# Kernel tuning notes

Hardware: AMD Instinct MI355X
Metric: run time of the kernel (lower is better)

Reference implementation:

```python
import jax, jax.numpy as jnp
import numpy as np

N_NODES = 50000
NEG_SLOPE = 0.2  # PyG GATConv default
EPS = 1e-16      # PyG softmax eps


def gat_conv(x, src, dst, W, a_s, a_d, b, n_nodes):
    """One PyG-style GATConv layer (concat heads). a_s/a_d: [H, C]."""
    H, C = a_s.shape
    h = (x @ W).reshape(n_nodes, H, C)                   # [N, H, C]
    al_s = jnp.sum(h * a_s[None], axis=-1)               # [N, H]
    al_d = jnp.sum(h * a_d[None], axis=-1)               # [N, H]
    e = jax.nn.leaky_relu(al_s[src] + al_d[dst], NEG_SLOPE)  # [E, H]
    # segment softmax over incoming edges of each destination node
    m = jax.ops.segment_max(e, dst, num_segments=n_nodes)
    m = jnp.where(jnp.isfinite(m), m, 0.0)
    ex = jnp.exp(e - m[dst])
    denom = jax.ops.segment_sum(ex, dst, num_segments=n_nodes)
    alpha = ex / (denom[dst] + EPS)                       # [E, H]
    out = jax.ops.segment_sum(alpha[:, :, None] * h[src], dst, num_segments=n_nodes)
    return out.reshape(n_nodes, H * C) + b                # concat heads + bias


def setup_inputs() -> dict:
    key = jax.random.key(0)
    ks = jax.random.split(key, 16)
    s = 0.05
    return {
        "x": jax.random.normal(ks[0], (N_NODES, 256), jnp.float32),
        "edge_index": jax.random.randint(ks[1], (2, 800000), 0, N_NODES, jnp.int64),
        "W1": jax.random.normal(ks[2], (256, 256), jnp.float32) * s,
        "as1": jax.random.normal(ks[3], (4, 64), jnp.float32) * s,
        "ad1": jax.random.normal(ks[4], (4, 64), jnp.float32) * s,
        "b1": jnp.zeros((256,), jnp.float32),
        "W2": jax.random.normal(ks[5], (256, 256), jnp.float32) * s,
        "as2": jax.random.normal(ks[6], (4, 64), jnp.float32) * s,
        "ad2": jax.random.normal(ks[7], (4, 64), jnp.float32) * s,
        "b2": jnp.zeros((256,), jnp.float32),
        "W3": jax.random.normal(ks[8], (256, 128), jnp.float32) * s,
        "as3": jax.random.normal(ks[9], (1, 128), jnp.float32) * s,
        "ad3": jax.random.normal(ks[10], (1, 128), jnp.float32) * s,
        "b3": jnp.zeros((128,), jnp.float32),
    }


def reference(x, edge_index, W1, as1, ad1, b1, W2, as2, ad2, b2, W3, as3, ad3, b3):
    n = x.shape[0]
    loop = jnp.arange(n, dtype=edge_index.dtype)
    src = jnp.concatenate([edge_index[0], loop])  # add_self_loops=True (PyG default)
    dst = jnp.concatenate([edge_index[1], loop])
    # F.dropout(p=0.6, training=False) -> identity in eval
    h = gat_conv(x, src, dst, W1, as1, ad1, b1, n)
    h = jax.nn.elu(h)  # gnn_act='elu'
    h = gat_conv(h, src, dst, W2, as2, ad2, b2, n)
    h = jax.nn.elu(h)
    h = gat_conv(h, src, dst, W3, as3, ad3, b3, n)
    return h
```

## Files before the change

### kernel.cpp

```cpp
#include <hip/hip_runtime.h>
#include <math.h>


#define NEG_SLOPE 0.2f
#define EPS_SM 1e-16f

typedef _Float16 half8 __attribute__((ext_vector_type(8)));
typedef _Float16 half4v __attribute__((ext_vector_type(4)));
typedef _Float16 half2v __attribute__((ext_vector_type(2)));
typedef float f32x4 __attribute__((ext_vector_type(4)));

__device__ __forceinline__ float wave_allred_sum(float v) {
#pragma unroll
    for (int o = 32; o > 0; o >>= 1) v += __shfl_xor(v, o, 64);
    return v;
}
__device__ __forceinline__ float4 lrelu4(float4 v) {
    v.x = (v.x < 0.f) ? NEG_SLOPE * v.x : v.x;
    v.y = (v.y < 0.f) ? NEG_SLOPE * v.y : v.y;
    v.z = (v.z < 0.f) ? NEG_SLOPE * v.z : v.z;
    v.w = (v.w < 0.f) ? NEG_SLOPE * v.w : v.w;
    return v;
}

__global__ void hist_kernel(const int* __restrict__ ei, int E, int N,
                            int* __restrict__ cnt) {
    int e = blockIdx.x * 256 + threadIdx.x;
    int ET = E + N;
    if (e >= ET) return;
    int dst = (e < E) ? ei[E + e] : (e - E);
    atomicAdd(&cnt[dst], 1);
}

__global__ void scan_block(const int* __restrict__ cnt, int n_cnt,
                           int* __restrict__ offs, int n_off,
                           int* __restrict__ bsums) {
    __shared__ int buf[1024];
    int gid = blockIdx.x * 1024 + threadIdx.x;
    int v = (gid < n_cnt) ? cnt[gid] : 0;
    buf[threadIdx.x] = v;
    __syncthreads();
#pragma unroll
    for (int off = 1; off < 1024; off <<= 1) {
        int t = (threadIdx.x >= off) ? buf[threadIdx.x - off] : 0;
        __syncthreads();
        buf[threadIdx.x] += t;
        __syncthreads();
    }
    if (gid < n_off) offs[gid] = buf[threadIdx.x] - v;
    if (threadIdx.x == 1023) bsums[blockIdx.x] = buf[1023];
}

__global__ void scan_sums(int* __restrict__ bsums, int nb) {
    int l = threadIdx.x;
    int v = (l < nb) ? bsums[l] : 0;
    int s = v;
#pragma unroll
    for (int o = 1; o < 64; o <<= 1) {
        int t = __shfl_up(s, o, 64);
        if (l >= o) s += t;
    }
    if (l < nb) bsums[l] = s - v;
}

__global__ void scan_add(int* __restrict__ offs, int n_off,
                         const int* __restrict__ bsums) {
    int gid = blockIdx.x * 1024 + threadIdx.x;
    if (gid < n_off) offs[gid] += bsums[blockIdx.x];
}

__global__ void fill_csr(const int* __restrict__ ei, int E, int N,
                         const int* __restrict__ offs, int* __restrict__ fil,
                         int* __restrict__ csr) {
    int e = blockIdx.x * 256 + threadIdx.x;
    int ET = E + N;
    if (e >= ET) return;
    int src, dst;
    if (e < E) { src = ei[e]; dst = ei[E + e]; }
    else       { src = dst = e - E; }
    int pos = offs[dst] + atomicAdd(&fil[dst], 1);
    csr[pos] = src;
}

__global__ void wcast_all(const float* __restrict__ W1,
                          const float* __restrict__ W2,
                          const float* __restrict__ W3,
                          _Float16* __restrict__ o1,
                          _Float16* __restrict__ o2,
                          _Float16* __restrict__ o3) {
    int i = blockIdx.x * 256 + threadIdx.x;
    const float* W; _Float16* o; int K = 256, N, s;
    if (i < 65536)        { W = W1; o = o1; N = 256; s = i; }
    else if (i < 131072)  { W = W2; o = o2; N = 256; s = i - 65536; }
    else if (i < 163840)  { W = W3; o = o3; N = 128; s = i - 131072; }
    else return;
    int n = s / K, k = s - n * K;
    o[s] = (_Float16)W[(size_t)k * N + n];
}

template <bool AF32, int ALMODE>
__global__ __launch_bounds__(256) void gemm_f16(
    const void* __restrict__ Ain, const _Float16* __restrict__ Bt,
    _Float16* __restrict__ C,
    const float* __restrict__ a_s, const float* __restrict__ a_d,
    float* __restrict__ als, float* __restrict__ ald,
    int M, int N, int K) {
    __shared__ _Float16 As[2][128][40], Bs[2][128][40];
    __shared__ float s_als[128], s_ald[128];
    const int bm = blockIdx.y * 128, bn = blockIdx.x * 128;
    const int tid = threadIdx.x;
    const int w = tid >> 6, lane = tid & 63;
    const int wm = (w >> 1) * 64, wn = (w & 1) * 64;
    const int l16 = lane & 15, q = lane >> 4;
    const int kq = q * 8;
    const int sr = tid >> 1;
    const int sk = (tid & 1) * 16;
    const int row = bm + sr;
    const int NT = K >> 5;

    f32x4 acc[4][4];
#pragma unroll
    for (int i = 0; i < 4; ++i)
#pragma unroll
        for (int j = 0; j < 4; ++j) acc[i][j] = (f32x4){0.f, 0.f, 0.f, 0.f};

    half8 ra0, ra1, rb0, rb1;
    auto LOAD = [&](int kt) {
        if constexpr (AF32) {
            const float* Af = (const float*)Ain;
            float4 v0, v1, v2, v3;
            if (row < M) {
                const float4* ap = (const float4*)(Af + (size_t)row * K + kt + sk);
                v0 = ap[0]; v1 = ap[1]; v2 = ap[2]; v3 = ap[3];
            } else {
                v0 = v1 = v2 = v3 = make_float4(0.f, 0.f, 0.f, 0.f);
            }
            ra0[0] = (_Float16)v0.x; ra0[1] = (_Float16)v0.y;
            ra0[2] = (_Float16)v0.z; ra0[3] = (_Float16)v0.w;
            ra0[4] = (_Float16)v1.x; ra0[5] = (_Float16)v1.y;
            ra0[6] = (_Float16)v1.z; ra0[7] = (_Float16)v1.w;
            ra1[0] = (_Float16)v2.x; ra1[1] = (_Float16)v2.y;
            ra1[2] = (_Float16)v2.z; ra1[3] = (_Float16)v2.w;
            ra1[4] = (_Float16)v3.x; ra1[5] = (_Float16)v3.y;
            ra1[6] = (_Float16)v3.z; ra1[7] = (_Float16)v3.w;
        } else {
            const _Float16* Ah = (const _Float16*)Ain;
            if (row < M) {
                const half8* ap = (const half8*)(Ah + (size_t)row * K + kt + sk);
                ra0 = ap[0]; ra1 = ap[1];
            } else {
                ra0 = (half8)(_Float16)0; ra1 = (half8)(_Float16)0;
            }
        }
        const half8* bp = (const half8*)(Bt + (size_t)(bn + sr) * K + kt + sk);
        rb0 = bp[0]; rb1 = bp[1];
    };
    auto STORE = [&](int nb) {
        *(half8*)&As[nb][sr][sk]     = ra0;
        *(half8*)&As[nb][sr][sk + 8] = ra1;
        *(half8*)&Bs[nb][sr][sk]     = rb0;
        *(half8*)&Bs[nb][sr][sk + 8] = rb1;
    };

    LOAD(0);
    STORE(0);
    int cur = 0;
    for (int kb = 0; kb < NT; ++kb) {
        const bool more = (kb + 1) < NT;
        if (more) LOAD((kb + 1) * 32);
        __syncthreads();
        half8 a[4], b[4];
#pragma unroll
        for (int t = 0; t < 4; ++t) {
            a[t] = *(const half8*)&As[cur][wm + t * 16 + l16][kq];
            b[t] = *(const half8*)&Bs[cur][wn + t * 16 + l16][kq];
        }
#pragma unroll
        for (int i = 0; i < 4; ++i)
#pragma unroll
            for (int j = 0; j < 4; ++j)
                acc[i][j] = __builtin_amdgcn_mfma_f32_16x16x32_f16(
                    a[i], b[j], acc[i][j], 0, 0, 0);
        if (more) STORE(cur ^ 1);
        cur ^= 1;
    }

    if constexpr (ALMODE == 2) {
        __syncthreads();
        if (tid < 128) { s_als[tid] = 0.f; s_ald[tid] = 0.f; }
        __syncthreads();
    }
#pragma unroll
    for (int i = 0; i < 4; ++i) {
#pragma unroll
        for (int r = 0; r < 4; ++r) {
            int orow = bm + wm + i * 16 + q * 4 + r;
            float c0 = acc[i][0][r], c1 = acc[i][1][r];
            float c2 = acc[i][2][r], c3 = acc[i][3][r];
            if (orow < M) {
                _Float16* cp = C + (size_t)orow * N + bn + wn + l16;
                cp[0]  = (_Float16)c0;
                cp[16] = (_Float16)c1;
                cp[32] = (_Float16)c2;
                cp[48] = (_Float16)c3;
            }
            {
                const int cg = bn + wn + l16;
                float ps = c0 * a_s[cg] + c1 * a_s[cg + 16] +
                           c2 * a_s[cg + 32] + c3 * a_s[cg + 48];
                float pd = c0 * a_d[cg] + c1 * a_d[cg + 16] +
                           c2 * a_d[cg + 32] + c3 * a_d[cg + 48];
#pragma unroll
                for (int o = 1; o < 16; o <<= 1) {
                    ps += __shfl_xor(ps, o, 64);
                    pd += __shfl_xor(pd, o, 64);
                }
                if constexpr (ALMODE == 1) {
                    if (l16 == 0 && orow < M) {
                        const int head = (bn + wn) >> 6;
                        als[orow * 4 + head] = ps;
                        ald[orow * 4 + head] = pd;
                    }
                } else {
                    if (l16 == 0) {
                        atomicAdd(&s_als[wm + i * 16 + q * 4 + r], ps);
                        atomicAdd(&s_ald[wm + i * 16 + q * 4 + r], pd);
                    }
                }
            }
        }
    }
    if constexpr (ALMODE == 2) {
        __syncthreads();
        if (tid < 128) {
            int orow = bm + tid;
            if (orow < M) { als[orow] = s_als[tid]; ald[orow] = s_ald[tid]; }
        }
    }
}

template <bool ACT>
__global__ __launch_bounds__(256) void aggregate_h4_f16(
    const _Float16* __restrict__ h, const float4* __restrict__ als4,
    const float4* __restrict__ ald4, const int* __restrict__ offs,
    const int* __restrict__ csr, const float* __restrict__ bias,
    _Float16* __restrict__ out, int Nn) {
    const int tid = threadIdx.x;
    const int w = tid >> 6;
    const int l = tid & 63;
    const int n = blockIdx.x * 4 + w;
    __shared__ float s_alpha[4][64][4];
    __shared__ int s_src[4][64];
    if (n >= Nn) return;

    const int base = offs[n];
    const int deg = offs[n + 1] - base;
    const float4 adv = ald4[n];
    const int head = l >> 4;

    float4 acc = make_float4(0.f, 0.f, 0.f, 0.f);
    float4 den = make_float4(0.f, 0.f, 0.f, 0.f);
    for (int c0 = 0; c0 < deg; c0 += 64) {
        const int cl = min(64, deg - c0);
        if (l < cl) {
            int s = csr[base + c0 + l];
            float4 a = als4[s];
            float4 sc = lrelu4(make_float4(a.x + adv.x, a.y + adv.y,
                                           a.z + adv.z, a.w + adv.w));
            float4 ex = make_float4(__expf(sc.x), __expf(sc.y),
                                    __expf(sc.z), __expf(sc.w));
            *(float4*)&s_alpha[w][l][0] = ex;
            s_src[w][l] = s;
            den.x += ex.x; den.y += ex.y; den.z += ex.z; den.w += ex.w;
        }
        int e = 0;
        for (; e + 4 <= cl; e += 4) {
            int s0 = s_src[w][e + 0], s1 = s_src[w][e + 1];
            int s2 = s_src[w][e + 2], s3 = s_src[w][e + 3];
            float a0 = s_alpha[w][e + 0][head];
            float a1 = s_alpha[w][e + 1][head];
            float a2 = s_alpha[w][e + 2][head];
            float a3 = s_alpha[w][e + 3][head];
            half4v hv0 = *(const half4v*)(h + (size_t)s0 * 256 + l * 4);
            half4v hv1 = *(const half4v*)(h + (size_t)s1 * 256 + l * 4);
            half4v hv2 = *(const half4v*)(h + (size_t)s2 * 256 + l * 4);
            half4v hv3 = *(const half4v*)(h + (size_t)s3 * 256 + l * 4);
            acc.x = fmaf(a0, (float)hv0[0], acc.x);
            acc.y = fmaf(a0, (float)hv0[1], acc.y);
            acc.z = fmaf(a0, (float)hv0[2], acc.z);
            acc.w = fmaf(a0, (float)hv0[3], acc.w);
            acc.x = fmaf(a1, (float)hv1[0], acc.x);
            acc.y = fmaf(a1, (float)hv1[1], acc.y);
            acc.z = fmaf(a1, (float)hv1[2], acc.z);
            acc.w = fmaf(a1, (float)hv1[3], acc.w);
            acc.x = fmaf(a2, (float)hv2[0], acc.x);
            acc.y = fmaf(a2, (float)hv2[1], acc.y);
            acc.z = fmaf(a2, (float)hv2[2], acc.z);
            acc.w = fmaf(a2, (float)hv2[3], acc.w);
            acc.x = fmaf(a3, (float)hv3[0], acc.x);
            acc.y = fmaf(a3, (float)hv3[1], acc.y);
            acc.z = fmaf(a3, (float)hv3[2], acc.z);
            acc.w = fmaf(a3, (float)hv3[3], acc.w);
        }
        for (; e < cl; ++e) {
            int s0 = s_src[w][e];
            float a0 = s_alpha[w][e][head];
            half4v hv0 = *(const half4v*)(h + (size_t)s0 * 256 + l * 4);
            acc.x = fmaf(a0, (float)hv0[0], acc.x);
            acc.y = fmaf(a0, (float)hv0[1], acc.y);
            acc.z = fmaf(a0, (float)hv0[2], acc.z);
            acc.w = fmaf(a0, (float)hv0[3], acc.w);
        }
    }
    den.x = wave_allred_sum(den.x); den.y = wave_allred_sum(den.y);
    den.z = wave_allred_sum(den.z); den.w = wave_allred_sum(den.w);
    float d = (head == 0) ? den.x : (head == 1) ? den.y
             : (head == 2) ? den.z : den.w;
    const float rc = 1.f / (d + EPS_SM);

    float4 bv = *(const float4*)(bias + l * 4);
    float4 r = make_float4(acc.x * rc + bv.x, acc.y * rc + bv.y,
                           acc.z * rc + bv.z, acc.w * rc + bv.w);
    if (ACT) {
        r.x = (r.x > 0.f) ? r.x : expm1f(r.x);
        r.y = (r.y > 0.f) ? r.y : expm1f(r.y);
        r.z = (r.z > 0.f) ? r.z : expm1f(r.z);
        r.w = (r.w > 0.f) ? r.w : expm1f(r.w);
    }
    half4v ov = {(_Float16)r.x, (_Float16)r.y, (_Float16)r.z, (_Float16)r.w};
    *(half4v*)(out + (size_t)n * 256 + l * 4) = ov;
}

__global__ __launch_bounds__(256) void aggregate_h1_f16(
    const _Float16* __restrict__ h, const float* __restrict__ als,
    const float* __restrict__ ald, const int* __restrict__ offs,
    const int* __restrict__ csr, const float* __restrict__ bias,
    float* __restrict__ out, int Nn) {
    const int tid = threadIdx.x;
    const int w = tid >> 6;
    const int l = tid & 63;
    const int n = blockIdx.x * 4 + w;
    __shared__ float s_alpha[4][64];
    __shared__ int s_src[4][64];
    if (n >= Nn) return;

    const int base = offs[n];
    const int deg = offs[n + 1] - base;
    const float ad_n = ald[n];

    float2 acc = make_float2(0.f, 0.f);
    float den = 0.f;
    for (int c0 = 0; c0 < deg; c0 += 64) {
        const int cl = min(64, deg - c0);
        if (l < cl) {
            int s = csr[base + c0 + l];
            float sc = als[s] + ad_n;
            sc = (sc < 0.f) ? NEG_SLOPE * sc : sc;
            float ex = __expf(sc);
            s_alpha[w][l] = ex;
            s_src[w][l] = s;
            den += ex;
        }
        int e = 0;
        for (; e + 4 <= cl; e += 4) {
            int s0 = s_src[w][e + 0], s1 = s_src[w][e + 1];
            int s2 = s_src[w][e + 2], s3 = s_src[w][e + 3];
            float a0 = s_alpha[w][e + 0], a1 = s_alpha[w][e + 1];
            float a2 = s_alpha[w][e + 2], a3 = s_alpha[w][e + 3];
            half2v v0 = *(const half2v*)(h + (size_t)s0 * 128 + l * 2);
            half2v v1 = *(const half2v*)(h + (size_t)s1 * 128 + l * 2);
            half2v v2 = *(const half2v*)(h + (size_t)s2 * 128 + l * 2);
            half2v v3 = *(const half2v*)(h + (size_t)s3 * 128 + l * 2);
            acc.x = fmaf(a0, (float)v0[0], acc.x); acc.y = fmaf(a0, (float)v0[1], acc.y);
            acc.x = fmaf(a1, (float)v1[0], acc.x); acc.y = fmaf(a1, (float)v1[1], acc.y);
            acc.x = fmaf(a2, (float)v2[0], acc.x); acc.y = fmaf(a2, (float)v2[1], acc.y);
            acc.x = fmaf(a3, (float)v3[0], acc.x); acc.y = fmaf(a3, (float)v3[1], acc.y);
        }
        for (; e < cl; ++e) {
            int s0 = s_src[w][e];
            float a0 = s_alpha[w][e];
            half2v v0 = *(const half2v*)(h + (size_t)s0 * 128 + l * 2);
            acc.x = fmaf(a0, (float)v0[0], acc.x); acc.y = fmaf(a0, (float)v0[1], acc.y);
        }
    }
    den = wave_allred_sum(den);
    const float rc = 1.f / (den + EPS_SM);
    float2 r = make_float2(acc.x * rc + bias[l * 2],
                           acc.y * rc + bias[l * 2 + 1]);
    *(float2*)(out + (size_t)n * 128 + l * 2) = r;
}

extern "C" void kernel_launch(void* const* d_in, const int* in_sizes, int n_in,
                              void* d_out, int out_size, void* d_ws,
                              size_t ws_size, hipStream_t stream) {
    const float* x   = (const float*)d_in[0];
    const int*   ei  = (const int*)d_in[1];
    const float* W1  = (const float*)d_in[2];
    const float* as1 = (const float*)d_in[3];
    const float* ad1 = (const float*)d_in[4];
    const float* b1  = (const float*)d_in[5];
    const float* W2  = (const float*)d_in[6];
    const float* as2 = (const float*)d_in[7];
    const float* ad2 = (const float*)d_in[8];
    const float* b2  = (const float*)d_in[9];
    const float* W3  = (const float*)d_in[10];
    const float* as3 = (const float*)d_in[11];
    const float* ad3 = (const float*)d_in[12];
    const float* b3  = (const float*)d_in[13];

    const int Nn = in_sizes[0] / 256;
    const int E  = in_sizes[1] / 2;
    const int ET = E + Nn;

    char* p = (char*)d_ws;
    _Float16* bufA = (_Float16*)p; p += (size_t)Nn * 256 * 2;
    _Float16* bufB = (_Float16*)p; p += (size_t)Nn * 256 * 2;
    float* als  = (float*)p; p += (size_t)Nn * 4 * 4;
    float* ald  = (float*)p; p += (size_t)Nn * 4 * 4;
    int* cnt  = (int*)p; p += (size_t)Nn * 4;
    int* fil  = (int*)p; p += (size_t)Nn * 4;
    int* offs = (int*)p; p += (size_t)(Nn + 1) * 4;
    int* bsums = (int*)p; p += 256 * 4;
    int* csr  = (int*)p; p += (size_t)ET * 4;
    p = (char*)(((uintptr_t)p + 15) & ~(uintptr_t)15);
    _Float16* wt1 = (_Float16*)p; p += 256 * 256 * 2;
    _Float16* wt2 = (_Float16*)p; p += 256 * 256 * 2;
    _Float16* wt3 = (_Float16*)p; p += 128 * 256 * 2;

    hipMemsetAsync(cnt, 0, (size_t)2 * Nn * sizeof(int), stream);
    int nbE = (ET + 255) / 256;
    hist_kernel<<<nbE, 256, 0, stream>>>(ei, E, Nn, cnt);
    wcast_all<<<(163840 + 255) / 256, 256, 0, stream>>>(W1, W2, W3, wt1, wt2, wt3);
    int nbS = (Nn + 1 + 1023) / 1024;
    scan_block<<<nbS, 1024, 0, stream>>>(cnt, Nn, offs, Nn + 1, bsums);
    scan_sums<<<1, 64, 0, stream>>>(bsums, nbS);
    scan_add<<<nbS, 1024, 0, stream>>>(offs, Nn + 1, bsums);
    fill_csr<<<nbE, 256, 0, stream>>>(ei, E, Nn, offs, fil, csr);

    const int gm = (Nn + 127) / 128;
    const int ga = (Nn + 3) / 4;

    gemm_f16<true, 1><<<dim3(2, gm), 256, 0, stream>>>(
        x, wt1, bufB, as1, ad1, als, ald, Nn, 256, 256);
    aggregate_h4_f16<true><<<ga, 256, 0, stream>>>(
        bufB, (const float4*)als, (const float4*)ald, offs, csr, b1, bufA, Nn);

    gemm_f16<false, 1><<<dim3(2, gm), 256, 0, stream>>>(
        bufA, wt2, bufB, as2, ad2, als, ald, Nn, 256, 256);
    aggregate_h4_f16<true><<<ga, 256, 0, stream>>>(
        bufB, (const float4*)als, (const float4*)ald, offs, csr, b2, bufA, Nn);

    gemm_f16<false, 2><<<dim3(1, gm), 256, 0, stream>>>(
        bufA, wt3, bufB, as3, ad3, als, ald, Nn, 128, 256);
    aggregate_h1_f16<<<ga, 256, 0, stream>>>(
        bufB, als, ald, offs, csr, b3, (float*)d_out, Nn);
}
```

Baseline: 435.0 us.

## Split aggregation across column slices with edge-parallel lane groups

The aggregation kernels now launch four blocks per node group, each handling one 64-column slice (one head) or a 32-column slice in the last layer. Within a wave, lane groups process different edges in parallel and are combined by cross-lane shuffle reductions. The intent is more parallelism and more independent gathers in flight per wave, raising memory-level parallelism for the gather-bound step. In exchange, the CSR index and attention-logit work is repeated for each slice, and the kernels add shuffle reductions and idle lanes at the final write.

```diff
diff --git a/kernel.cpp b/kernel.cpp
--- a/kernel.cpp
+++ b/kernel.cpp
@@ -7,19 +7,11 @@
 
 typedef _Float16 half8 __attribute__((ext_vector_type(8)));
 typedef _Float16 half4v __attribute__((ext_vector_type(4)));
-typedef _Float16 half2v __attribute__((ext_vector_type(2)));
 typedef float f32x4 __attribute__((ext_vector_type(4)));
 
 __device__ __forceinline__ float wave_allred_sum(float v) {
 #pragma unroll
     for (int o = 32; o > 0; o >>= 1) v += __shfl_xor(v, o, 64);
-    return v;
-}
-__device__ __forceinline__ float4 lrelu4(float4 v) {
-    v.x = (v.x < 0.f) ? NEG_SLOPE * v.x : v.x;
-    v.y = (v.y < 0.f) ? NEG_SLOPE * v.y : v.y;
-    v.z = (v.z < 0.f) ? NEG_SLOPE * v.z : v.z;
-    v.w = (v.w < 0.f) ? NEG_SLOPE * v.w : v.w;
     return v;
 }
 
@@ -240,98 +232,94 @@
 }
 
 template <bool ACT>
-__global__ __launch_bounds__(256) void aggregate_h4_f16(
-    const _Float16* __restrict__ h, const float4* __restrict__ als4,
-    const float4* __restrict__ ald4, const int* __restrict__ offs,
+__global__ __launch_bounds__(256) void aggregate_h4_sliced(
+    const _Float16* __restrict__ h, const float* __restrict__ als,
+    const float* __restrict__ ald, const int* __restrict__ offs,
     const int* __restrict__ csr, const float* __restrict__ bias,
     _Float16* __restrict__ out, int Nn) {
     const int tid = threadIdx.x;
     const int w = tid >> 6;
     const int l = tid & 63;
-    const int n = blockIdx.x * 4 + w;
-    __shared__ float s_alpha[4][64][4];
+    const int slice = blockIdx.x & 3;
+    const int n = (blockIdx.x >> 2) * 4 + w;
+    __shared__ float s_alpha[4][64];
     __shared__ int s_src[4][64];
     if (n >= Nn) return;
 
     const int base = offs[n];
     const int deg = offs[n + 1] - base;
-    const float4 adv = ald4[n];
-    const int head = l >> 4;
-
-    float4 acc = make_float4(0.f, 0.f, 0.f, 0.f);
-    float4 den = make_float4(0.f, 0.f, 0.f, 0.f);
-    for (int c0 = 0; c0 < deg; c0 += 64) {
-        const int cl = min(64, deg - c0);
-        if (l < cl) {
-            int s = csr[base + c0 + l];
-            float4 a = als4[s];
-            float4 sc = lrelu4(make_float4(a.x + adv.x, a.y + adv.y,
-                                           a.z + adv.z, a.w + adv.w));
-            float4 ex = make_float4(__expf(sc.x), __expf(sc.y),
-                                    __expf(sc.z), __expf(sc.w));
-            *(float4*)&s_alpha[w][l][0] = ex;
+    const float adn = ald[n * 4 + slice];
+    const int g = l >> 4;
+    const int cq = l & 15;
+    const int col = slice * 64 + cq * 4;
+
+    float den = 0.f;
+    float4 acc0 = make_float4(0.f, 0.f, 0.f, 0.f);
+    float4 acc1 = make_float4(0.f, 0.f, 0.f, 0.f);
+    for (int b0 = 0; b0 < deg; b0 += 64) {
+        const int bl = min(64, deg - b0);
+        if (l < bl) {
+            int s = csr[base + b0 + l];
+            float a = als[s * 4 + slice] + adn;
+            a = (a < 0.f) ? NEG_SLOPE * a : a;
+            float ex = __expf(a);
+            s_alpha[w][l] = ex;
             s_src[w][l] = s;
-            den.x += ex.x; den.y += ex.y; den.z += ex.z; den.w += ex.w;
-        }
-        int e = 0;
-        for (; e + 4 <= cl; e += 4) {
-            int s0 = s_src[w][e + 0], s1 = s_src[w][e + 1];
-            int s2 = s_src[w][e + 2], s3 = s_src[w][e + 3];
-            float a0 = s_alpha[w][e + 0][head];
-            float a1 = s_alpha[w][e + 1][head];
-            float a2 = s_alpha[w][e + 2][head];
-            float a3 = s_alpha[w][e + 3][head];
-            half4v hv0 = *(const half4v*)(h + (size_t)s0 * 256 + l * 4);
-            half4v hv1 = *(const half4v*)(h + (size_t)s1 * 256 + l * 4);
-            half4v hv2 = *(const half4v*)(h + (size_t)s2 * 256 + l * 4);
-            half4v hv3 = *(const half4v*)(h + (size_t)s3 * 256 + l * 4);
-            acc.x = fmaf(a0, (float)hv0[0], acc.x);
-            acc.y = fmaf(a0, (float)hv0[1], acc.y);
-            acc.z = fmaf(a0, (float)hv0[2], acc.z);
-            acc.w = fmaf(a0, (float)hv0[3], acc.w);
-            acc.x = fmaf(a1, (float)hv1[0], acc.x);
-            acc.y = fmaf(a1, (float)hv1[1], acc.y);
-            acc.z = fmaf(a1, (float)hv1[2], acc.z);
-            acc.w = fmaf(a1, (float)hv1[3], acc.w);
-            acc.x = fmaf(a2, (float)hv2[0], acc.x);
-            acc.y = fmaf(a2, (float)hv2[1], acc.y);
-            acc.z = fmaf(a2, (float)hv2[2], acc.z);
-            acc.w = fmaf(a2, (float)hv2[3], acc.w);
-            acc.x = fmaf(a3, (float)hv3[0], acc.x);
-            acc.y = fmaf(a3, (float)hv3[1], acc.y);
-            acc.z = fmaf(a3, (float)hv3[2], acc.z);
-            acc.w = fmaf(a3, (float)hv3[3], acc.w);
-        }
-        for (; e < cl; ++e) {
+            den += ex;
+        }
+        int e = g;
+        for (; e + 4 < bl; e += 8) {
+            int s0 = s_src[w][e], s1 = s_src[w][e + 4];
+            float a0 = s_alpha[w][e], a1 = s_alpha[w][e + 4];
+            half4v v0 = *(const half4v*)(h + (size_t)s0 * 256 + col);
+            half4v v1 = *(const half4v*)(h + (size_t)s1 * 256 + col);
+            acc0.x = fmaf(a0, (float)v0[0], acc0.x);
+            acc0.y = fmaf(a0, (float)v0[1], acc0.y);
+            acc0.z = fmaf(a0, (float)v0[2], acc0.z);
+            acc0.w = fmaf(a0, (float)v0[3], acc0.w);
+            acc1.x = fmaf(a1, (float)v1[0], acc1.x);
+            acc1.y = fmaf(a1, (float)v1[1], acc1.y);
+            acc1.z = fmaf(a1, (float)v1[2], acc1.z);
+            acc1.w = fmaf(a1, (float)v1[3], acc1.w);
+        }
+        if (e < bl) {
             int s0 = s_src[w][e];
-            float a0 = s_alpha[w][e][head];
-            half4v hv0 = *(const half4v*)(h + (size_t)s0 * 256 + l * 4);
-            acc.x = fmaf(a0, (float)hv0[0], acc.x);
-            acc.y = fmaf(a0, (float)hv0[1], acc.y);
-            acc.z = fmaf(a0, (float)hv0[2], acc.z);
-            acc.w = fmaf(a0, (float)hv0[3], acc.w);
-        }
-    }
-    den.x = wave_allred_sum(den.x); den.y = wave_allred_sum(den.y);
-    den.z = wave_allred_sum(den.z); den.w = wave_allred_sum(den.w);
-    float d = (head == 0) ? den.x : (head == 1) ? den.y
-             : (head == 2) ? den.z : den.w;
-    const float rc = 1.f / (d + EPS_SM);
-
-    float4 bv = *(const float4*)(bias + l * 4);
-    float4 r = make_float4(acc.x * rc + bv.x, acc.y * rc + bv.y,
-                           acc.z * rc + bv.z, acc.w * rc + bv.w);
-    if (ACT) {
-        r.x = (r.x > 0.f) ? r.x : expm1f(r.x);
-        r.y = (r.y > 0.f) ? r.y : expm1f(r.y);
-        r.z = (r.z > 0.f) ? r.z : expm1f(r.z);
-        r.w = (r.w > 0.f) ? r.w : expm1f(r.w);
-    }
-    half4v ov = {(_Float16)r.x, (_Float16)r.y, (_Float16)r.z, (_Float16)r.w};
-    *(half4v*)(out + (size_t)n * 256 + l * 4) = ov;
-}
-
-__global__ __launch_bounds__(256) void aggregate_h1_f16(
+            float a0 = s_alpha[w][e];
+            half4v v0 = *(const half4v*)(h + (size_t)s0 * 256 + col);
+            acc0.x = fmaf(a0, (float)v0[0], acc0.x);
+            acc0.y = fmaf(a0, (float)v0[1], acc0.y);
+            acc0.z = fmaf(a0, (float)v0[2], acc0.z);
+            acc0.w = fmaf(a0, (float)v0[3], acc0.w);
+        }
+    }
+    float4 acc = make_float4(acc0.x + acc1.x, acc0.y + acc1.y,
+                             acc0.z + acc1.z, acc0.w + acc1.w);
+#pragma unroll
+    for (int o = 16; o < 64; o <<= 1) {
+        acc.x += __shfl_xor(acc.x, o, 64);
+        acc.y += __shfl_xor(acc.y, o, 64);
+        acc.z += __shfl_xor(acc.z, o, 64);
+        acc.w += __shfl_xor(acc.w, o, 64);
+    }
+    den = wave_allred_sum(den);
+    const float rc = 1.f / (den + EPS_SM);
+
+    if (g == 0) {
+        float4 bv = *(const float4*)(bias + col);
+        float4 r = make_float4(acc.x * rc + bv.x, acc.y * rc + bv.y,
+                               acc.z * rc + bv.z, acc.w * rc + bv.w);
+        if (ACT) {
+            r.x = (r.x > 0.f) ? r.x : expm1f(r.x);
+            r.y = (r.y > 0.f) ? r.y : expm1f(r.y);
+            r.z = (r.z > 0.f) ? r.z : expm1f(r.z);
+            r.w = (r.w > 0.f) ? r.w : expm1f(r.w);
+        }
+        half4v ov = {(_Float16)r.x, (_Float16)r.y, (_Float16)r.z, (_Float16)r.w};
+        *(half4v*)(out + (size_t)n * 256 + col) = ov;
+    }
+}
+
+__global__ __launch_bounds__(256) void aggregate_h1_sliced(
     const _Float16* __restrict__ h, const float* __restrict__ als,
     const float* __restrict__ ald, const int* __restrict__ offs,
     const int* __restrict__ csr, const float* __restrict__ bias,
@@ -339,55 +327,76 @@
     const int tid = threadIdx.x;
     const int w = tid >> 6;
     const int l = tid & 63;
-    const int n = blockIdx.x * 4 + w;
+    const int slice = blockIdx.x & 3;
+    const int n = (blockIdx.x >> 2) * 4 + w;
     __shared__ float s_alpha[4][64];
     __shared__ int s_src[4][64];
     if (n >= Nn) return;
 
     const int base = offs[n];
     const int deg = offs[n + 1] - base;
-    const float ad_n = ald[n];
-
-    float2 acc = make_float2(0.f, 0.f);
+    const float adn = ald[n];
+    const int g = l >> 3;
+    const int cq = l & 7;
+    const int col = slice * 32 + cq * 4;
+
     float den = 0.f;
-    for (int c0 = 0; c0 < deg; c0 += 64) {
-        const int cl = min(64, deg - c0);
-        if (l < cl) {
-            int s = csr[base + c0 + l];
-            float sc = als[s] + ad_n;
-            sc = (sc < 0.f) ? NEG_SLOPE * sc : sc;
-            float ex = __expf(sc);
+    float4 acc0 = make_float4(0.f, 0.f, 0.f, 0.f);
+    float4 acc1 = make_float4(0.f, 0.f, 0.f, 0.f);
+    for (int b0 = 0; b0 < deg; b0 += 64) {
+        const int bl = min(64, deg - b0);
+        if (l < bl) {
+            int s = csr[base + b0 + l];
+            float a = als[s] + adn;
+            a = (a < 0.f) ? NEG_SLOPE * a : a;
+            float ex = __expf(a);
             s_alpha[w][l] = ex;
             s_src[w][l] = s;
             den += ex;
         }
-        int e = 0;
-        for (; e + 4 <= cl; e += 4) {
-            int s0 = s_src[w][e + 0], s1 = s_src[w][e + 1];
-            int s2 = s_src[w][e + 2], s3 = s_src[w][e + 3];
-            float a0 = s_alpha[w][e + 0], a1 = s_alpha[w][e + 1];
-            float a2 = s_alpha[w][e + 2], a3 = s_alpha[w][e + 3];
-            half2v v0 = *(const half2v*)(h + (size_t)s0 * 128 + l * 2);
-            half2v v1 = *(const half2v*)(h + (size_t)s1 * 128 + l * 2);
-            half2v v2 = *(const half2v*)(h + (size_t)s2 * 128 + l * 2);
-            half2v v3 = *(const half2v*)(h + (size_t)s3 * 128 + l * 2);
-            acc.x = fmaf(a0, (float)v0[0], acc.x); acc.y = fmaf(a0, (float)v0[1], acc.y);
-            acc.x = fmaf(a1, (float)v1[0], acc.x); acc.y = fmaf(a1, (float)v1[1], acc.y);
-            acc.x = fmaf(a2, (float)v2[0], acc.x); acc.y = fmaf(a2, (float)v2[1], acc.y);
-            acc.x = fmaf(a3, (float)v3[0], acc.x); acc.y = fmaf(a3, (float)v3[1], acc.y);
-        }
-        for (; e < cl; ++e) {
+        int e = g;
+        for (; e + 8 < bl; e += 16) {
+            int s0 = s_src[w][e], s1 = s_src[w][e + 8];
+            float a0 = s_alpha[w][e], a1 = s_alpha[w][e + 8];
+            half4v v0 = *(const half4v*)(h + (size_t)s0 * 128 + col);
+            half4v v1 = *(const half4v*)(h + (size_t)s1 * 128 + col);
+            acc0.x = fmaf(a0, (float)v0[0], acc0.x);
+            acc0.y = fmaf(a0, (float)v0[1], acc0.y);
+            acc0.z = fmaf(a0, (float)v0[2], acc0.z);
+            acc0.w = fmaf(a0, (float)v0[3], acc0.w);
+            acc1.x = fmaf(a1, (float)v1[0], acc1.x);
+            acc1.y = fmaf(a1, (float)v1[1], acc1.y);
+            acc1.z = fmaf(a1, (float)v1[2], acc1.z);
+            acc1.w = fmaf(a1, (float)v1[3], acc1.w);
+        }
+        if (e < bl) {
             int s0 = s_src[w][e];
             float a0 = s_alpha[w][e];
-            half2v v0 = *(const half2v*)(h + (size_t)s0 * 128 + l * 2);
-            acc.x = fmaf(a0, (float)v0[0], acc.x); acc.y = fmaf(a0, (float)v0[1], acc.y);
-        }
+            half4v v0 = *(const half4v*)(h + (size_t)s0 * 128 + col);
+            acc0.x = fmaf(a0, (float)v0[0], acc0.x);
+            acc0.y = fmaf(a0, (float)v0[1], acc0.y);
+            acc0.z = fmaf(a0, (float)v0[2], acc0.z);
+            acc0.w = fmaf(a0, (float)v0[3], acc0.w);
+        }
+    }
+    float4 acc = make_float4(acc0.x + acc1.x, acc0.y + acc1.y,
+                             acc0.z + acc1.z, acc0.w + acc1.w);
+#pragma unroll
+    for (int o = 8; o < 64; o <<= 1) {
+        acc.x += __shfl_xor(acc.x, o, 64);
+        acc.y += __shfl_xor(acc.y, o, 64);
+        acc.z += __shfl_xor(acc.z, o, 64);
+        acc.w += __shfl_xor(acc.w, o, 64);
     }
     den = wave_allred_sum(den);
     const float rc = 1.f / (den + EPS_SM);
-    float2 r = make_float2(acc.x * rc + bias[l * 2],
-                           acc.y * rc + bias[l * 2 + 1]);
-    *(float2*)(out + (size_t)n * 128 + l * 2) = r;
+
+    if (g == 0) {
+        float4 bv = *(const float4*)(bias + col);
+        float4 r = make_float4(acc.x * rc + bv.x, acc.y * rc + bv.y,
+                               acc.z * rc + bv.z, acc.w * rc + bv.w);
+        *(float4*)(out + (size_t)n * 128 + col) = r;
+    }
 }
 
 extern "C" void kernel_launch(void* const* d_in, const int* in_sizes, int n_in,
@@ -438,20 +447,20 @@
     fill_csr<<<nbE, 256, 0, stream>>>(ei, E, Nn, offs, fil, csr);
 
     const int gm = (Nn + 127) / 128;
-    const int ga = (Nn + 3) / 4;
+    const int gaS = ((Nn + 3) / 4) * 4;
 
     gemm_f16<true, 1><<<dim3(2, gm), 256, 0, stream>>>(
         x, wt1, bufB, as1, ad1, als, ald, Nn, 256, 256);
-    aggregate_h4_f16<true><<<ga, 256, 0, stream>>>(
-        bufB, (const float4*)als, (const float4*)ald, offs, csr, b1, bufA, Nn);
+    aggregate_h4_sliced<true><<<gaS, 256, 0, stream>>>(
+        bufB, als, ald, offs, csr, b1, bufA, Nn);
 
     gemm_f16<false, 1><<<dim3(2, gm), 256, 0, stream>>>(
         bufA, wt2, bufB, as2, ad2, als, ald, Nn, 256, 256);
-    aggregate_h4_f16<true><<<ga, 256, 0, stream>>>(
-        bufB, (const float4*)als, (const float4*)ald, offs, csr, b2, bufA, Nn);
+    aggregate_h4_sliced<true><<<gaS, 256, 0, stream>>>(
+        bufB, als, ald, offs, csr, b2, bufA, Nn);
 
     gemm_f16<false, 2><<<dim3(1, gm), 256, 0, stream>>>(
         bufA, wt3, bufB, as3, ad3, als, ald, Nn, 128, 256);
-    aggregate_h1_f16<<<ga, 256, 0, stream>>>(
+    aggregate_h1_sliced<<<gaS, 256, 0, stream>>>(
         bufB, als, ald, offs, csr, b3, (float*)d_out, Nn);
 }
```

Measured after the change: 540.7 us. +24.3%, slower.
